# Kernel optimization log

Hardware: AMD Instinct MI355X
Metric: run time of the kernel (lower is better)

Reference implementation:

```python
import jax, jax.numpy as jnp
import numpy as np

NUM_GROUPS = 32
EPS = 1e-6


def group_norm(x, gamma, beta):
    # x: (B, C, H, W), 32 groups, eps=1e-6, affine
    B, C, H, W = x.shape
    xg = x.reshape(B, NUM_GROUPS, C // NUM_GROUPS, H, W)
    mean = xg.mean(axis=(2, 3, 4), keepdims=True)
    var = xg.var(axis=(2, 3, 4), keepdims=True)
    xn = ((xg - mean) * jax.lax.rsqrt(var + EPS)).reshape(B, C, H, W)
    return xn * gamma[None, :, None, None] + beta[None, :, None, None]


def conv1x1(x, w, b):
    # 1x1 conv == channel matmul. x: (B,C,H,W), w: (O,C), b: (O,)
    return jnp.einsum('bchw,oc->bohw', x, w) + b[None, :, None, None]


def setup_inputs() -> dict:
    key = jax.random.key(0)
    B, C, H, W = 16, 512, 32, 32
    ks = jax.random.split(key, 12)
    s = 1.0 / np.sqrt(C)
    return {
        'x': jax.random.normal(ks[0], (B, C, H, W), dtype=jnp.float32),
        'gn_gamma': jnp.ones((C,), dtype=jnp.float32),
        'gn_beta': jnp.zeros((C,), dtype=jnp.float32),
        'wq': jax.random.normal(ks[1], (C, C), dtype=jnp.float32) * s,
        'bq': jnp.zeros((C,), dtype=jnp.float32),
        'wk': jax.random.normal(ks[2], (C, C), dtype=jnp.float32) * s,
        'bk': jnp.zeros((C,), dtype=jnp.float32),
        'wv': jax.random.normal(ks[3], (C, C), dtype=jnp.float32) * s,
        'bv': jnp.zeros((C,), dtype=jnp.float32),
        'wp': jax.random.normal(ks[4], (C, C), dtype=jnp.float32) * s,
        'bp': jnp.zeros((C,), dtype=jnp.float32),
    }


def reference(x, gn_gamma, gn_beta, wq, bq, wk, bk, wv, bv, wp, bp):
    B, C, H, W = x.shape
    residual = x
    xn = group_norm(x, gn_gamma, gn_beta)
    q = conv1x1(xn, wq, bq).reshape(B, C, H * W)  # (B, C, HW)
    k = conv1x1(xn, wk, bk).reshape(B, C, H * W)
    v = conv1x1(xn, wv, bv).reshape(B, C, H * W)
    scale = C ** (-0.5)
    # energy[b,i,j] = q_i . k_j
    energy = jnp.einsum('bci,bcj->bij', q, k) * scale
    attn = jax.nn.softmax(energy, axis=-1)
    # out[b,c,i] = sum_j attn[b,i,j] * v[b,c,j]
    out = jnp.einsum('bij,bcj->bci', attn, v).reshape(B, C, H, W)
    out = conv1x1(out, wp, bp)
    return out + residual
```

## Files before the change

### kernel.cpp

```cpp
#include <hip/hip_runtime.h>
#include <hip/hip_bf16.h>

using bf16 = __hip_bfloat16;

typedef __attribute__((ext_vector_type(8))) __bf16 bf16x8;
typedef __attribute__((ext_vector_type(4))) float floatx4;

#define EPS 1e-6f

#define RAW_BARRIER()  asm volatile("s_barrier" ::: "memory")
#define WAIT_VM16()    asm volatile("s_waitcnt vmcnt(16)" ::: "memory")
#define WAIT_VM8()     asm volatile("s_waitcnt vmcnt(8)" ::: "memory")
#define WAIT_VM4()     asm volatile("s_waitcnt vmcnt(4)" ::: "memory")
#define WAIT_VM0()     asm volatile("s_waitcnt vmcnt(0)" ::: "memory")
#define PRIO1()        __builtin_amdgcn_s_setprio(1)
#define PRIO0()        __builtin_amdgcn_s_setprio(0)

__device__ __forceinline__ void load_lds16(const void* g, void* l) {
    __builtin_amdgcn_global_load_lds(
        (const __attribute__((address_space(1))) void*)g,
        (__attribute__((address_space(3))) void*)l, 16, 0, 0);
}

__device__ __forceinline__ void storeOut(float* p, float v) { *p = v; }
__device__ __forceinline__ void storeOut(bf16* p, float v) { *p = __float2bfloat16(v); }

#define MFMA16(a, b, c) __builtin_amdgcn_mfma_f32_16x16x32_bf16(a, b, c, 0, 0, 0)

template <int BIAS_MODE, int RESID_EN, int QKV, typename OutT>
__global__ __launch_bounds__(256, 2) void gemm2b(
    const bf16* __restrict__ A, long long aStride, int lda,
    const bf16* __restrict__ B, long long bStride, int ldb,
    OutT* __restrict__ D, long long dStride, int ldd,
    bf16* __restrict__ vout, long long vStride,
    const float* __restrict__ bias,
    const float* __restrict__ resid, long long rStride, int ldr,
    int K, int tpb, int gx)
{
    constexpr int HB = 8192;
    extern __shared__ char smem[];

    const unsigned chunk = gridDim.x >> 3;
    const unsigned glob  = (blockIdx.x & 7) * chunk + (blockIdx.x >> 3);
    const unsigned z  = glob / (unsigned)tpb;
    const unsigned t  = glob % (unsigned)tpb;
    const int m0 = (int)(t / (unsigned)gx) << 7;
    const int n0 = (int)(t % (unsigned)gx) << 7;

    const int tid  = threadIdx.x;
    const int lane = tid & 63;
    const int wave = tid >> 6;
    const int wm   = wave >> 1;
    const int wn   = wave & 1;

    const bf16* Ab = A + (size_t)z * aStride + (size_t)m0 * lda;
    const bf16* Bb = B + (size_t)z * bStride + (size_t)n0 * ldb;

    floatx4 acc[4][4];
#pragma unroll
    for (int i = 0; i < 4; ++i)
#pragma unroll
        for (int j = 0; j < 4; ++j) acc[i][j] = (floatx4){0.f, 0.f, 0.f, 0.f};

    const int laneRow = lane & 15;
    const int laneKq  = lane >> 4;
    const int kqs16   = (laneKq ^ ((laneRow >> 1) & 3)) << 4;
    const int arow0   = wm * 64 + laneRow;
    const int brow0   = wn * 64 + laneRow;

    auto stage = [&](int kt, int h) {
        char* Adst = smem + ((kt & 1) * 2 + h) * HB;
        char* Bdst = smem + 4 * HB + ((kt & 1) * 2 + h) * HB;
        const int kb = (kt << 6) + (h << 5);
#pragma unroll
        for (int u = 0; u < 2; ++u) {
            const int idx = tid + u * 256;
            const int r  = idx >> 2;
            const int qs = (idx & 3) ^ ((idx >> 3) & 3);
            load_lds16(Ab + (size_t)r * lda + kb + qs * 8, Adst + idx * 16);
        }
#pragma unroll
        for (int u = 0; u < 2; ++u) {
            const int idx = tid + u * 256;
            const int r  = idx >> 2;
            const int qs = (idx & 3) ^ ((idx >> 3) & 3);
            load_lds16(Bb + (size_t)r * ldb + kb + qs * 8, Bdst + idx * 16);
        }
    };

    const int nt = K >> 6;
    stage(0, 0); stage(0, 1); stage(1, 0);

    for (int kt = 0; kt < nt; ++kt) {
        const char* Ablk = smem + (kt & 1) * 2 * HB;
        const char* Bblk = smem + 4 * HB + (kt & 1) * 2 * HB;
        const bool lastT = (kt == nt - 1);

        if (lastT) WAIT_VM4(); else WAIT_VM8();
        RAW_BARRIER();
        bf16x8 af[4], bfr[4];
#pragma unroll
        for (int im = 0; im < 4; ++im)
            af[im] = *(const bf16x8*)(Ablk + (arow0 + im * 16) * 64 + kqs16);
#pragma unroll
        for (int in = 0; in < 4; ++in)
            bfr[in] = *(const bf16x8*)(Bblk + (brow0 + in * 16) * 64 + kqs16);
        if (kt + 1 < nt) stage(kt + 1, 1);
        RAW_BARRIER();
        PRIO1();
#pragma unroll
        for (int im = 0; im < 4; ++im)
#pragma unroll
            for (int in = 0; in < 4; ++in)
                acc[im][in] = MFMA16(af[im], bfr[in], acc[im][in]);
        PRIO0();

        if (lastT) WAIT_VM0(); else WAIT_VM8();
        RAW_BARRIER();
#pragma unroll
        for (int im = 0; im < 4; ++im)
            af[im] = *(const bf16x8*)(Ablk + HB + (arow0 + im * 16) * 64 + kqs16);
#pragma unroll
        for (int in = 0; in < 4; ++in)
            bfr[in] = *(const bf16x8*)(Bblk + HB + (brow0 + in * 16) * 64 + kqs16);
        if (kt + 2 < nt) stage(kt + 2, 0);
        RAW_BARRIER();
        PRIO1();
#pragma unroll
        for (int im = 0; im < 4; ++im)
#pragma unroll
            for (int in = 0; in < 4; ++in)
                acc[im][in] = MFMA16(af[im], bfr[in], acc[im][in]);
        PRIO0();
    }

    const size_t dbase = (size_t)z * dStride;
#pragma unroll
    for (int im = 0; im < 4; ++im) {
        const int gmb = m0 + wm * 64 + im * 16 + (laneKq << 2);
#pragma unroll
        for (int in = 0; in < 4; ++in) {
            const int gn = n0 + wn * 64 + in * 16 + laneRow;
            float bn = 0.f;
            if (BIAS_MODE == 2) bn = bias[gn];
            if (QKV && n0 >= 1024) {
                union { bf16 h[4]; ushort4 u; } pk;
#pragma unroll
                for (int r = 0; r < 4; ++r)
                    pk.h[r] = __float2bfloat16(acc[im][in][r] + bn);
                *(ushort4*)(vout + (size_t)z * vStride +
                            (size_t)(gn - 1024) * 1024 + gmb) = pk.u;
            } else {
#pragma unroll
                for (int r = 0; r < 4; ++r) {
                    const int gm = gmb + r;
                    float v = acc[im][in][r];
                    if (BIAS_MODE == 1) v += bias[gm];
                    if (BIAS_MODE == 2) v += bn;
                    if (RESID_EN)
                        v += resid[(size_t)z * rStride + (size_t)gm * ldr + gn];
                    storeOut(D + dbase + (size_t)gm * ldd + gn, v);
                }
            }
        }
    }
}

__global__ __launch_bounds__(256, 1) void fattn(
    const bf16* __restrict__ qkT,
    const bf16* __restrict__ vv,
    bf16* __restrict__ O2,
    float scale)
{
    constexpr int KT = 32768;
    extern __shared__ char smem[];
    __shared__ __align__(16) char plds[4 * 1024];

    const int bid  = blockIdx.x;
    const int glob = (bid & 7) * 32 + (bid >> 3);
    const int b    = glob >> 4;
    const int i0   = (glob & 15) << 6;

    const int tid     = threadIdx.x;
    const int lane    = tid & 63;
    const int wave    = tid >> 6;
    const int laneRow = lane & 15;
    const int laneKq  = lane >> 4;
    const int kqs16   = (laneKq ^ ((laneRow >> 1) & 3)) << 4;

    const bf16* Qb = qkT + (size_t)b * 1048576 + (size_t)(i0 + wave * 16) * 1024;
    const bf16* Kb = qkT + (size_t)b * 1048576 + 512;
    const bf16* Vb = vv + (size_t)b * 524288;

    bf16x8 qf[16];
#pragma unroll
    for (int ks = 0; ks < 16; ++ks)
        qf[ks] = *(const bf16x8*)(Qb + (size_t)laneRow * 1024 + ks * 32 + laneKq * 8);

    floatx4 acc[32];
#pragma unroll
    for (int mf = 0; mf < 32; ++mf) acc[mf] = (floatx4){0.f, 0.f, 0.f, 0.f};
    float rs = 0.f;

    auto stageK = [&](int jt) {
        char* dst = smem + (jt & 1) * KT;
        const bf16* src = Kb + ((size_t)jt << 5) * 1024;
#pragma unroll
        for (int u = 0; u < 8; ++u) {
            const int idx = tid + u * 256;
            const int kk = idx >> 7;
            const int j  = (idx >> 2) & 31;
            const int p  = idx & 3;
            load_lds16(src + (size_t)j * 1024 + kk * 32 + 8 * (p ^ ((j >> 1) & 3)),
                       dst + idx * 16);
        }
    };
    auto stageV = [&](int jt) {
        char* dst = smem + 2 * KT + (jt & 1) * KT;
        const bf16* src = Vb + (jt << 5);
#pragma unroll
        for (int u = 0; u < 8; ++u) {
            const int idx = tid + u * 256;
            const int c = idx >> 2;
            const int p = idx & 3;
            load_lds16(src + (size_t)c * 1024 + 8 * (p ^ ((c >> 1) & 3)),
                       dst + idx * 16);
        }
    };

    stageK(0); stageV(0); stageK(1); stageV(1);

    char* pl = plds + wave * 1024 + laneRow * 64;
    const int sw2 = ((laneRow >> 1) & 3) << 1;

    for (int jt = 0; jt < 32; ++jt) {
        if (jt == 31) WAIT_VM0(); else WAIT_VM16();
        RAW_BARRIER();
        const char* Kt = smem + (jt & 1) * KT;
        const char* Vt = smem + 2 * KT + (jt & 1) * KT;

        floatx4 s0 = (floatx4){0.f, 0.f, 0.f, 0.f};
        floatx4 s1 = (floatx4){0.f, 0.f, 0.f, 0.f};
#pragma unroll
        for (int ks = 0; ks < 16; ++ks) {
            bf16x8 kf0 = *(const bf16x8*)(Kt + ks * 2048 + laneRow * 64 + kqs16);
            bf16x8 kf1 = *(const bf16x8*)(Kt + ks * 2048 + (laneRow + 16) * 64 + kqs16);
            s0 = MFMA16(kf0, qf[ks], s0);
            s1 = MFMA16(kf1, qf[ks], s1);
        }

        union { bf16 h[4]; unsigned long long u; } w0, w1;
#pragma unroll
        for (int r = 0; r < 4; ++r) {
            float v0 = __expf(s0[r] * scale);
            float v1 = __expf(s1[r] * scale);
            rs += v0 + v1;
            w0.h[r] = __float2bfloat16(v0);
            w1.h[r] = __float2bfloat16(v1);
        }
        *(unsigned long long*)(pl + ((laneKq)     ^ sw2) * 8) = w0.u;
        *(unsigned long long*)(pl + ((laneKq + 4) ^ sw2) * 8) = w1.u;
        asm volatile("s_waitcnt lgkmcnt(0)" ::: "memory");
        __builtin_amdgcn_sched_barrier(0);
        bf16x8 pf = *(const bf16x8*)(pl + kqs16);

        PRIO1();
#pragma unroll
        for (int mf = 0; mf < 32; ++mf) {
            bf16x8 vf = *(const bf16x8*)(Vt + (laneRow + 16 * mf) * 64 + kqs16);
            acc[mf] = MFMA16(vf, pf, acc[mf]);
        }
        PRIO0();

        RAW_BARRIER();
        if (jt + 2 < 32) { stageK(jt + 2); stageV(jt + 2); }
    }

    rs += __shfl_xor(rs, 16);
    rs += __shfl_xor(rs, 32);
    const float ri = 1.f / rs;

    bf16* Ob = O2 + (size_t)b * 524288 +
               (size_t)(i0 + wave * 16 + laneRow) * 512 + (laneKq << 2);
#pragma unroll
    for (int mf = 0; mf < 32; ++mf) {
        union { bf16 h[4]; ushort4 u; } pk;
#pragma unroll
        for (int r = 0; r < 4; ++r)
            pk.h[r] = __float2bfloat16(acc[mf][r] * ri);
        *(ushort4*)(Ob + mf * 16) = pk.u;
    }
}

__global__ __launch_bounds__(256) void gn_stats(const float* __restrict__ x,
                                                float* __restrict__ stats)
{
    const int bg = blockIdx.x;
    const float4* p = (const float4*)(x + (size_t)bg * 16384);
    float s = 0.f, ss = 0.f;
    for (int i = threadIdx.x; i < 4096; i += 256) {
        float4 v = p[i];
        s  += v.x + v.y + v.z + v.w;
        ss += v.x * v.x + v.y * v.y + v.z * v.z + v.w * v.w;
    }
#pragma unroll
    for (int off = 32; off; off >>= 1) {
        s  += __shfl_down(s, off);
        ss += __shfl_down(ss, off);
    }
    __shared__ float rs[4], rss[4];
    const int wv = threadIdx.x >> 6;
    if ((threadIdx.x & 63) == 0) { rs[wv] = s; rss[wv] = ss; }
    __syncthreads();
    if (threadIdx.x == 0) {
        float S  = rs[0] + rs[1] + rs[2] + rs[3];
        float SS = rss[0] + rss[1] + rss[2] + rss[3];
        float mean = S * (1.f / 16384.f);
        float var  = SS * (1.f / 16384.f) - mean * mean;
        stats[2 * bg]     = mean;
        stats[2 * bg + 1] = rsqrtf(var + EPS);
    }
}

__global__ __launch_bounds__(256) void gn_apply_t(const float* __restrict__ x,
                                                  const float* __restrict__ stats,
                                                  const float* __restrict__ gamma,
                                                  const float* __restrict__ beta,
                                                  bf16* __restrict__ xnT)
{
    __shared__ bf16 tile[32][36];
    const int b = blockIdx.z, c0 = blockIdx.y * 32, i0 = blockIdx.x * 32;
    {
        const int cc = threadIdx.x >> 3;
        const int i4 = (threadIdx.x & 7) << 2;
        const int c  = c0 + cc;
        const float mean = stats[2 * ((b << 5) + (c >> 4))];
        const float rstd = stats[2 * ((b << 5) + (c >> 4)) + 1];
        const float a  = gamma[c] * rstd;
        const float bb = beta[c] - mean * a;
        float4 v = *(const float4*)(x + (((size_t)(b * 512 + c)) << 10) + i0 + i4);
        tile[cc][i4 + 0] = __float2bfloat16(v.x * a + bb);
        tile[cc][i4 + 1] = __float2bfloat16(v.y * a + bb);
        tile[cc][i4 + 2] = __float2bfloat16(v.z * a + bb);
        tile[cc][i4 + 3] = __float2bfloat16(v.w * a + bb);
    }
    __syncthreads();
    {
        const int ii = threadIdx.x >> 3;
        const int c4 = (threadIdx.x & 7) << 2;
        union { bf16 h[4]; uint2 u; } pk;
        pk.h[0] = tile[c4 + 0][ii];
        pk.h[1] = tile[c4 + 1][ii];
        pk.h[2] = tile[c4 + 2][ii];
        pk.h[3] = tile[c4 + 3][ii];
        *((uint2*)(xnT + (((size_t)(b * 1024 + i0 + ii)) << 9) + c0 + c4)) = pk.u;
    }
}

__global__ __launch_bounds__(256) void prep(
    const float* __restrict__ wq, const float* __restrict__ wk,
    const float* __restrict__ wv, const float* __restrict__ wp,
    bf16* __restrict__ wqkvb, bf16* __restrict__ wpb,
    const float* __restrict__ bq, const float* __restrict__ bk,
    const float* __restrict__ bv, float* __restrict__ bqkv)
{
    const int id = blockIdx.x;
    if (id < 1024) {
        const int w = id >> 8;
        const float* src = (w == 0) ? wq : (w == 1) ? wk : (w == 2) ? wv : wp;
        bf16* dst = (w < 3) ? (wqkvb + (size_t)w * 262144) : wpb;
        const int g = (id & 255) * 256 + threadIdx.x;
        float4 v = ((const float4*)src)[g];
        union { bf16 h[4]; uint2 u; } pk;
        pk.h[0] = __float2bfloat16(v.x);
        pk.h[1] = __float2bfloat16(v.y);
        pk.h[2] = __float2bfloat16(v.z);
        pk.h[3] = __float2bfloat16(v.w);
        ((uint2*)dst)[g] = pk.u;
    } else {
        for (int t = threadIdx.x; t < 1536; t += 256)
            bqkv[t] = (t < 512) ? bq[t] : (t < 1024) ? bk[t - 512] : bv[t - 1024];
    }
}

extern "C" void kernel_launch(void* const* d_in, const int* in_sizes, int n_in,
                              void* d_out, int out_size, void* d_ws, size_t ws_size,
                              hipStream_t stream)
{
    const float* x     = (const float*)d_in[0];
    const float* gamma = (const float*)d_in[1];
    const float* beta  = (const float*)d_in[2];
    const float* wq    = (const float*)d_in[3];
    const float* bq    = (const float*)d_in[4];
    const float* wk    = (const float*)d_in[5];
    const float* bk    = (const float*)d_in[6];
    const float* wv    = (const float*)d_in[7];
    const float* bv    = (const float*)d_in[8];
    const float* wp    = (const float*)d_in[9];
    const float* bp    = (const float*)d_in[10];
    float* out = (float*)d_out;

    char* ws = (char*)d_ws;
    size_t off = 0;
    auto alloc = [&](size_t bytes) -> char* {
        char* p = ws + off;
        off += (bytes + 255) & ~(size_t)255;
        return p;
    };

    const long long S  = 1024, C = 512;
    const long long BS = S * C;
    const long long ES = S * S;

    float* stats  = (float*)alloc(512 * 2 * sizeof(float));
    float* bqkv   = (float*)alloc(1536 * sizeof(float));
    bf16* wqkvb = (bf16*)alloc((size_t)3 * C * C * 2);
    bf16* wpb   = (bf16*)alloc((size_t)C * C * 2);
    bf16* xnT   = (bf16*)alloc((size_t)16 * BS * 2);
    bf16* qkT   = (bf16*)alloc((size_t)16 * ES * 2);
    bf16* vv    = (bf16*)alloc((size_t)16 * BS * 2);
    bf16* O2    = (bf16*)alloc((size_t)16 * BS * 2);

    hipFuncSetAttribute((const void*)gemm2b<2, 0, 1, bf16>,
                        hipFuncAttributeMaxDynamicSharedMemorySize, 65536);
    hipFuncSetAttribute((const void*)gemm2b<1, 1, 0, float>,
                        hipFuncAttributeMaxDynamicSharedMemorySize, 65536);
    hipFuncSetAttribute((const void*)fattn,
                        hipFuncAttributeMaxDynamicSharedMemorySize, 131072);

    prep<<<1025, 256, 0, stream>>>(wq, wk, wv, wp, wqkvb, wpb, bq, bk, bv, bqkv);

    gn_stats<<<512, 256, 0, stream>>>(x, stats);
    gn_apply_t<<<dim3(32, 16, 16), 256, 0, stream>>>(x, stats, gamma, beta, xnT);

    gemm2b<2, 0, 1, bf16><<<1536, 256, 65536, stream>>>(
        xnT, BS, 512, wqkvb, 0, 512, qkT, ES, 1024, vv, BS,
        bqkv, nullptr, 0, 0, 512, 96, 12);

    const float scale = 0.044194173824159216f;
    fattn<<<256, 256, 131072, stream>>>(qkT, vv, O2, scale);

    gemm2b<1, 1, 0, float><<<512, 256, 65536, stream>>>(
        wpb, 0, 512, O2, BS, 512, out, BS, 1024, nullptr, 0,
        bp, x, BS, 1024, 512, 32, 8);
}
```

Measured before the change: 254.2 us.

## Load V fragments straight to registers and triple-buffer K tiles in LDS

In the attention kernel, V tiles are no longer staged through LDS. Each wave now loads its 32 V fragments directly from global memory into registers at the start of each iteration, and waits on them with vmcnt just before the PV MFMAs. K staging moves to a three-slot LDS ring, which removes the second barrier per iteration and cuts dynamic LDS to 96 KB. The aim is to drop LDS traffic and a barrier from the loop. The cost is about 128 extra VGPRs per thread, with a risk of spills, and each of the four waves re-reads the same V tile from global memory or L2.

```diff
diff --git a/kernel.cpp b/kernel.cpp
--- a/kernel.cpp
+++ b/kernel.cpp
@@ -9,10 +9,10 @@
 #define EPS 1e-6f
 
 #define RAW_BARRIER()  asm volatile("s_barrier" ::: "memory")
-#define WAIT_VM16()    asm volatile("s_waitcnt vmcnt(16)" ::: "memory")
 #define WAIT_VM8()     asm volatile("s_waitcnt vmcnt(8)" ::: "memory")
 #define WAIT_VM4()     asm volatile("s_waitcnt vmcnt(4)" ::: "memory")
 #define WAIT_VM0()     asm volatile("s_waitcnt vmcnt(0)" ::: "memory")
+#define SCHED_FENCE()  __builtin_amdgcn_sched_barrier(0)
 #define PRIO1()        __builtin_amdgcn_s_setprio(1)
 #define PRIO0()        __builtin_amdgcn_s_setprio(0)
 
@@ -190,7 +190,7 @@
 
     const bf16* Qb = qkT + (size_t)b * 1048576 + (size_t)(i0 + wave * 16) * 1024;
     const bf16* Kb = qkT + (size_t)b * 1048576 + 512;
-    const bf16* Vb = vv + (size_t)b * 524288;
+    const bf16* Vb = vv + (size_t)b * 524288 + (size_t)laneRow * 1024 + laneKq * 8;
 
     bf16x8 qf[16];
 #pragma unroll
@@ -203,7 +203,7 @@
     float rs = 0.f;
 
     auto stageK = [&](int jt) {
-        char* dst = smem + (jt & 1) * KT;
+        char* dst = smem + (jt % 3) * KT;
         const bf16* src = Kb + ((size_t)jt << 5) * 1024;
 #pragma unroll
         for (int u = 0; u < 8; ++u) {
@@ -215,29 +215,25 @@
                        dst + idx * 16);
         }
     };
-    auto stageV = [&](int jt) {
-        char* dst = smem + 2 * KT + (jt & 1) * KT;
-        const bf16* src = Vb + (jt << 5);
-#pragma unroll
-        for (int u = 0; u < 8; ++u) {
-            const int idx = tid + u * 256;
-            const int c = idx >> 2;
-            const int p = idx & 3;
-            load_lds16(src + (size_t)c * 1024 + 8 * (p ^ ((c >> 1) & 3)),
-                       dst + idx * 16);
-        }
-    };
-
-    stageK(0); stageV(0); stageK(1); stageV(1);
+
+    stageK(0); stageK(1);
 
     char* pl = plds + wave * 1024 + laneRow * 64;
     const int sw2 = ((laneRow >> 1) & 3) << 1;
 
     for (int jt = 0; jt < 32; ++jt) {
-        if (jt == 31) WAIT_VM0(); else WAIT_VM16();
+        WAIT_VM8();
         RAW_BARRIER();
-        const char* Kt = smem + (jt & 1) * KT;
-        const char* Vt = smem + 2 * KT + (jt & 1) * KT;
+        const char* Kt = smem + (jt % 3) * KT;
+
+        bf16x8 vf[32];
+        const bf16* vsrc = Vb + (jt << 5);
+#pragma unroll
+        for (int mf = 0; mf < 32; ++mf)
+            vf[mf] = *(const bf16x8*)(vsrc + (size_t)mf * 16384);
+        SCHED_FENCE();
+        if (jt + 2 < 32) stageK(jt + 2);
+        SCHED_FENCE();
 
         floatx4 s0 = (floatx4){0.f, 0.f, 0.f, 0.f};
         floatx4 s1 = (floatx4){0.f, 0.f, 0.f, 0.f};
@@ -261,19 +257,16 @@
         *(unsigned long long*)(pl + ((laneKq)     ^ sw2) * 8) = w0.u;
         *(unsigned long long*)(pl + ((laneKq + 4) ^ sw2) * 8) = w1.u;
         asm volatile("s_waitcnt lgkmcnt(0)" ::: "memory");
-        __builtin_amdgcn_sched_barrier(0);
+        SCHED_FENCE();
         bf16x8 pf = *(const bf16x8*)(pl + kqs16);
 
+        if (jt >= 30) WAIT_VM0(); else WAIT_VM8();
+
         PRIO1();
 #pragma unroll
-        for (int mf = 0; mf < 32; ++mf) {
-            bf16x8 vf = *(const bf16x8*)(Vt + (laneRow + 16 * mf) * 64 + kqs16);
-            acc[mf] = MFMA16(vf, pf, acc[mf]);
-        }
+        for (int mf = 0; mf < 32; ++mf)
+            acc[mf] = MFMA16(vf[mf], pf, acc[mf]);
         PRIO0();
-
-        RAW_BARRIER();
-        if (jt + 2 < 32) { stageK(jt + 2); stageV(jt + 2); }
     }
 
     rs += __shfl_xor(rs, 16);
@@ -426,7 +419,7 @@
     hipFuncSetAttribute((const void*)gemm2b<1, 1, 0, float>,
                         hipFuncAttributeMaxDynamicSharedMemorySize, 65536);
     hipFuncSetAttribute((const void*)fattn,
-                        hipFuncAttributeMaxDynamicSharedMemorySize, 131072);
+                        hipFuncAttributeMaxDynamicSharedMemorySize, 98304);
 
     prep<<<1025, 256, 0, stream>>>(wq, wk, wv, wp, wqkvb, wpb, bq, bk, bv, bqkv);
 
@@ -438,7 +431,7 @@
         bqkv, nullptr, 0, 0, 512, 96, 12);
 
     const float scale = 0.044194173824159216f;
-    fattn<<<256, 256, 131072, stream>>>(qkT, vv, O2, scale);
+    fattn<<<256, 256, 98304, stream>>>(qkT, vv, O2, scale);
 
     gemm2b<1, 1, 0, float><<<512, 256, 65536, stream>>>(
         wpb, 0, 512, O2, BS, 512, out, BS, 1024, nullptr, 0,
```

New measurement: 338.7 us. +33.2%, slower.

## Split PV accumulation across waves by channel slice to reuse V fragments

Applied to the files above, without the earlier changes.

In the attention kernel, each wave used to compute all 512 output channels for its own 16 query rows, so every wave read the full V tile from LDS. Now each wave owns a 128-channel slice for all 64 query rows. It reads the P fragments of all four waves through LDS after an added barrier, and each V fragment is reused across four MFMAs. Row sums are exchanged through LDS for the final normalisation. The aim is to cut LDS traffic for V by a factor of four, at the cost of an extra block barrier per iteration and more P reads.

```diff
diff --git a/kernel.cpp b/kernel.cpp
--- a/kernel.cpp
+++ b/kernel.cpp
@@ -13,6 +13,7 @@
 #define WAIT_VM8()     asm volatile("s_waitcnt vmcnt(8)" ::: "memory")
 #define WAIT_VM4()     asm volatile("s_waitcnt vmcnt(4)" ::: "memory")
 #define WAIT_VM0()     asm volatile("s_waitcnt vmcnt(0)" ::: "memory")
+#define SCHED_FENCE()  __builtin_amdgcn_sched_barrier(0)
 #define PRIO1()        __builtin_amdgcn_s_setprio(1)
 #define PRIO0()        __builtin_amdgcn_s_setprio(0)
 
@@ -175,6 +176,7 @@
     constexpr int KT = 32768;
     extern __shared__ char smem[];
     __shared__ __align__(16) char plds[4 * 1024];
+    __shared__ float rsLDS[64];
 
     const int bid  = blockIdx.x;
     const int glob = (bid & 7) * 32 + (bid >> 3);
@@ -197,9 +199,11 @@
     for (int ks = 0; ks < 16; ++ks)
         qf[ks] = *(const bf16x8*)(Qb + (size_t)laneRow * 1024 + ks * 32 + laneKq * 8);
 
-    floatx4 acc[32];
-#pragma unroll
-    for (int mf = 0; mf < 32; ++mf) acc[mf] = (floatx4){0.f, 0.f, 0.f, 0.f};
+    floatx4 acc[8][4];
+#pragma unroll
+    for (int mf = 0; mf < 8; ++mf)
+#pragma unroll
+        for (int ni = 0; ni < 4; ++ni) acc[mf][ni] = (floatx4){0.f, 0.f, 0.f, 0.f};
     float rs = 0.f;
 
     auto stageK = [&](int jt) {
@@ -230,7 +234,7 @@
 
     stageK(0); stageV(0); stageK(1); stageV(1);
 
-    char* pl = plds + wave * 1024 + laneRow * 64;
+    char* plw = plds + wave * 1024 + laneRow * 64;
     const int sw2 = ((laneRow >> 1) & 3) << 1;
 
     for (int jt = 0; jt < 32; ++jt) {
@@ -258,17 +262,24 @@
             w0.h[r] = __float2bfloat16(v0);
             w1.h[r] = __float2bfloat16(v1);
         }
-        *(unsigned long long*)(pl + ((laneKq)     ^ sw2) * 8) = w0.u;
-        *(unsigned long long*)(pl + ((laneKq + 4) ^ sw2) * 8) = w1.u;
+        *(unsigned long long*)(plw + ((laneKq)     ^ sw2) * 8) = w0.u;
+        *(unsigned long long*)(plw + ((laneKq + 4) ^ sw2) * 8) = w1.u;
         asm volatile("s_waitcnt lgkmcnt(0)" ::: "memory");
-        __builtin_amdgcn_sched_barrier(0);
-        bf16x8 pf = *(const bf16x8*)(pl + kqs16);
+        RAW_BARRIER();
+        SCHED_FENCE();
+        bf16x8 pf[4];
+#pragma unroll
+        for (int ni = 0; ni < 4; ++ni)
+            pf[ni] = *(const bf16x8*)(plds + ni * 1024 + laneRow * 64 + kqs16);
 
         PRIO1();
 #pragma unroll
-        for (int mf = 0; mf < 32; ++mf) {
-            bf16x8 vf = *(const bf16x8*)(Vt + (laneRow + 16 * mf) * 64 + kqs16);
-            acc[mf] = MFMA16(vf, pf, acc[mf]);
+        for (int mf = 0; mf < 8; ++mf) {
+            bf16x8 vf = *(const bf16x8*)(Vt +
+                (wave * 128 + mf * 16 + laneRow) * 64 + kqs16);
+#pragma unroll
+            for (int ni = 0; ni < 4; ++ni)
+                acc[mf][ni] = MFMA16(vf, pf[ni], acc[mf][ni]);
         }
         PRIO0();
 
@@ -278,17 +289,23 @@
 
     rs += __shfl_xor(rs, 16);
     rs += __shfl_xor(rs, 32);
-    const float ri = 1.f / rs;
-
-    bf16* Ob = O2 + (size_t)b * 524288 +
-               (size_t)(i0 + wave * 16 + laneRow) * 512 + (laneKq << 2);
-#pragma unroll
-    for (int mf = 0; mf < 32; ++mf) {
-        union { bf16 h[4]; ushort4 u; } pk;
-#pragma unroll
-        for (int r = 0; r < 4; ++r)
-            pk.h[r] = __float2bfloat16(acc[mf][r] * ri);
-        *(ushort4*)(Ob + mf * 16) = pk.u;
+    if (lane < 16) rsLDS[wave * 16 + lane] = rs;
+    __syncthreads();
+
+#pragma unroll
+    for (int ni = 0; ni < 4; ++ni) {
+        const float ri = 1.f / rsLDS[ni * 16 + laneRow];
+        bf16* Ob = O2 + (size_t)b * 524288 +
+                   (size_t)(i0 + ni * 16 + laneRow) * 512 +
+                   wave * 128 + (laneKq << 2);
+#pragma unroll
+        for (int mf = 0; mf < 8; ++mf) {
+            union { bf16 h[4]; ushort4 u; } pk;
+#pragma unroll
+            for (int r = 0; r < 4; ++r)
+                pk.h[r] = __float2bfloat16(acc[mf][ni][r] * ri);
+            *(ushort4*)(Ob + mf * 16) = pk.u;
+        }
     }
 }
 
@@ -308,12 +325,12 @@
         s  += __shfl_down(s, off);
         ss += __shfl_down(ss, off);
     }
-    __shared__ float rs[4], rss[4];
+    __shared__ float rsm[4], rss[4];
     const int wv = threadIdx.x >> 6;
-    if ((threadIdx.x & 63) == 0) { rs[wv] = s; rss[wv] = ss; }
+    if ((threadIdx.x & 63) == 0) { rsm[wv] = s; rss[wv] = ss; }
     __syncthreads();
     if (threadIdx.x == 0) {
-        float S  = rs[0] + rs[1] + rs[2] + rs[3];
+        float S  = rsm[0] + rsm[1] + rsm[2] + rsm[3];
         float SS = rss[0] + rss[1] + rss[2] + rss[3];
         float mean = S * (1.f / 16384.f);
         float var  = SS * (1.f / 16384.f) - mean * mean;
```

Measured after the change: 238.5 us. 1.07x faster.
